# Kernel tuning notes

Measured on AMD Instinct MI355X. Metric: run time of the kernel, lower is better.

The kernel has to match this reference:

```python
import jax, jax.numpy as jnp
import numpy as np

EPS = 1e-14
RHO = 8.0


def _normalize(x):
    return x / jnp.linalg.norm(x, axis=-1, keepdims=True)


def setup_inputs() -> dict:
    key = jax.random.key(0)
    ks = jax.random.split(key, 12)
    B, D = 4096, 1024
    f = lambda k: _normalize(jax.random.normal(k, (B, D), dtype=jnp.float32))
    pos = lambda k: jax.random.uniform(k, (B, 1), dtype=jnp.float32, minval=0.1, maxval=1.0)
    return {
        "im_feat": f(ks[0]),
        "tt_feat": f(ks[1]),
        "rim_feat": f(ks[2]),
        "rtt_feat": f(ks[3]),
        "remote_u_im": pos(ks[4]),
        "remote_u_tt": pos(ks[5]),
        "loss1_im": pos(ks[6]),
        "loss1_tt": pos(ks[7]),
        "u_im": pos(ks[8]),
        "u_tt": pos(ks[9]),
        "logit_scale": 10.0 * jnp.ones((1,), dtype=jnp.float32),
        "offset": 0,
    }


def _pairwise_loss(rim, rtt, im, tt, logit_scale, offset):
    # features1 = remote, features2 = local (as in forward(): pairwise_loss(remote_features, features, ...))
    sim_image = rim @ tt.T                                  # [B1, B2]
    sim_text = rtt @ im.T                                   # [B1, B2]
    diag_sim = jnp.sum(rim * rtt, axis=-1, keepdims=True)   # [B1, 1]
    exp_im = jnp.exp((sim_image - diag_sim) * logit_scale)
    exp_tt = jnp.exp((sim_text - diag_sim) * logit_scale)
    B1, B2 = sim_image.shape
    # mask zeros the shifted diagonal: equivalent to subtracting the diagonal entry from the row sum
    cols = (jnp.arange(B1) + offset)[:, None]               # [B1, 1]
    rw_sum = B2 - 1 if B1 <= B2 else B2 * (B1 - 1) / B1
    loss_im = (jnp.sum(exp_im, axis=-1, keepdims=True)
               - jnp.take_along_axis(exp_im, cols, axis=1)) / rw_sum
    loss_tt = (jnp.sum(exp_tt, axis=-1, keepdims=True)
               - jnp.take_along_axis(exp_tt, cols, axis=1)) / rw_sum
    return loss_im, loss_tt


def reference(im_feat, tt_feat, rim_feat, rtt_feat, remote_u_im, remote_u_tt,
              loss1_im, loss1_tt, u_im, u_tt, logit_scale, offset):
    loss2_im, loss2_tt = _pairwise_loss(rim_feat, rtt_feat, im_feat, tt_feat, logit_scale, offset)
    pg1 = loss1_im / (u_im + EPS) + loss1_tt / (u_tt + EPS)
    pg2 = loss2_im / (remote_u_im + EPS) + loss2_tt / (remote_u_tt + EPS)
    loss = (jnp.mean(pg1) + jnp.mean(pg2)) / 2
    # multiply_tau branch
    ls = logit_scale[0]
    loss = loss / jax.lax.stop_gradient(ls)
    loss = loss + RHO / ls
    loss = loss + jnp.mean(jnp.log(u_im) + jnp.log(u_tt)) / 2 / ls
    return loss
```

## Files before the change

kernel.cpp:

```cpp
#include <hip/hip_runtime.h>
#include <hip/hip_bf16.h>

#define EPSF 1e-14f
#define RHOF 8.0f

typedef __attribute__((ext_vector_type(4))) float f32x4;
typedef __attribute__((ext_vector_type(2))) unsigned long long u64x2;

#define AS_GLOBAL __attribute__((address_space(1)))
#define AS_LDS    __attribute__((address_space(3)))


__global__ __launch_bounds__(256) void prep_fp8(
    const float* __restrict__ im,  const float* __restrict__ tt,
    const float* __restrict__ rim, const float* __restrict__ rtt,
    unsigned char* __restrict__ bIm,  unsigned char* __restrict__ bTt,
    unsigned char* __restrict__ bRim, unsigned char* __restrict__ bRtt,
    float* __restrict__ S_im, float* __restrict__ S_tt,
    float* __restrict__ diag, float* __restrict__ red,
    int D, int spm )
{
    __shared__ unsigned char L[8 * 1024];
    const int b = blockIdx.x;
    const int tid = threadIdx.x;
    const int nConv = 4 * spm;
    if (b < nConv) {
        int mIdx = b / spm;
        int slab = b - mIdx * spm;
        const float* src = (mIdx == 0) ? rim : (mIdx == 1) ? tt
                          : (mIdx == 2) ? rtt : im;
        unsigned char* dst = (mIdx == 0) ? bRim : (mIdx == 1) ? bTt
                            : (mIdx == 2) ? bRtt : bIm;
        const float* srow = src + (size_t)slab * 8 * D;
        const int n4 = (8 * D) >> 2;
        for (int idx = tid; idx < n4; idx += 256) {
            float4 v = *(const float4*)(srow + idx * 4);
            int pk = __builtin_amdgcn_cvt_pk_fp8_f32(v.x, v.y, 0, false);
            pk     = __builtin_amdgcn_cvt_pk_fp8_f32(v.z, v.w, pk, true);
            *(int*)&L[idx * 4] = pk;
        }
        __syncthreads();
        const int kTiles = D >> 6;
        const int rb = (slab * 8) >> 7;
        const int r0loc = (slab * 8) & 127;
        for (int g = tid; g < (D >> 1); g += 256) {
            int kb  = g >> 5;
            int rem = g & 31;
            int rl  = rem >> 2;
            int h   = rem & 3;
            int r   = slab * 8 + rl;
            int m   = (r >> 1) & 7;
            int g0  = (2 * h) ^ m;
            const unsigned char* lb = &L[rl * D + kb * 64];
            u64x2 o;
            o.x = *(const unsigned long long*)(lb + g0 * 8);
            o.y = *(const unsigned long long*)(lb + (g0 ^ 1) * 8);
            char* outp = (char*)dst
                       + ((size_t)(rb * kTiles + kb) * 512
                          + (size_t)(r0loc + rl) * 4 + h) * 16;
            *(u64x2*)outp = o;
        }
    } else {
        int db = b - nConv;
        if (db == 0 && tid < 8) red[tid] = 0.f;
        if (tid < 4) { S_im[db * 4 + tid] = 0.f; S_tt[db * 4 + tid] = 0.f; }
        int row  = db * 4 + (tid >> 6);
        int lane = tid & 63;
        const float* a = rim + (size_t)row * D;
        const float* c = rtt + (size_t)row * D;
        float s = 0.f;
        for (int k = lane * 4; k < D; k += 256) {
            float4 av = *(const float4*)(a + k);
            float4 cv = *(const float4*)(c + k);
            s += av.x * cv.x + av.y * cv.y + av.z * cv.z + av.w * cv.w;
        }
        #pragma unroll
        for (int m2 = 1; m2 < 64; m2 <<= 1) s += __shfl_xor(s, m2, 64);
        if (lane == 0) diag[row] = s;
    }
}

__global__ __launch_bounds__(256) void gemm_expsum(
    const unsigned char* __restrict__ A0, const unsigned char* __restrict__ B0,
    float* __restrict__ S0,
    const unsigned char* __restrict__ A1, const unsigned char* __restrict__ B1,
    float* __restrict__ S1,
    const float* __restrict__ logit_scale, const int* __restrict__ offset,
    int Bn, int D)
{
    const int z = blockIdx.z;
    const unsigned char* A = z ? A1 : A0;
    const unsigned char* B = z ? B1 : B0;
    float* S = z ? S1 : S0;

    __shared__ unsigned char As[8192];
    __shared__ unsigned char Bs[8192];

    const int tid  = threadIdx.x;
    const int wave = tid >> 6;
    const int lane = tid & 63;
    const int lo   = lane & 15;
    const int qd   = lane >> 4;
    const int m0   = (wave >> 1) * 64;
    const int n0   = (wave & 1) * 64;
    const int x2   = (lo >> 3) & 1;
    const int xq   = qd ^ ((lo >> 1) & 3);
    const int off0 = x2 * 32 + xq * 8;
    const int off1 = (1 - x2) * 32 + xq * 8;

    const int kTiles = D >> 6;
    const unsigned char* Atile = A + (size_t)blockIdx.y * kTiles * 8192;
    const unsigned char* Btile = B + (size_t)blockIdx.x * kTiles * 8192;

    f32x4 acc[4][4];
    #pragma unroll
    for (int i = 0; i < 4; ++i)
        #pragma unroll
        for (int j = 0; j < 4; ++j)
            acc[i][j] = (f32x4){0.f, 0.f, 0.f, 0.f};

    for (int kb = 0; kb < kTiles; ++kb) {
        #pragma unroll
        for (int j = 0; j < 4; ++j) {
            int goff = (j * 256 + tid) * 16;
            int loff = j * 4096 + wave * 1024;
            __builtin_amdgcn_global_load_lds(
                (const AS_GLOBAL unsigned int*)(Atile + goff),
                (AS_LDS unsigned int*)&As[loff], 16, 0, 0);
            __builtin_amdgcn_global_load_lds(
                (const AS_GLOBAL unsigned int*)(Btile + goff),
                (AS_LDS unsigned int*)&Bs[loff], 16, 0, 0);
        }
        __syncthreads();

        long af0[4], af1[4], bq0[4], bq1[4];
        #pragma unroll
        for (int t = 0; t < 4; ++t) {
            int ra = (m0 + 16 * t + lo) * 64;
            af0[t] = *(const long*)&As[ra + off0];
            af1[t] = *(const long*)&As[ra + off1];
            int rn = (n0 + 16 * t + lo) * 64;
            bq0[t] = *(const long*)&Bs[rn + off0];
            bq1[t] = *(const long*)&Bs[rn + off1];
        }
        #pragma unroll
        for (int ti = 0; ti < 4; ++ti)
            #pragma unroll
            for (int tj = 0; tj < 4; ++tj) {
                acc[ti][tj] = __builtin_amdgcn_mfma_f32_16x16x32_fp8_fp8(
                    af0[ti], bq0[tj], acc[ti][tj], 0, 0, 0);
                acc[ti][tj] = __builtin_amdgcn_mfma_f32_16x16x32_fp8_fp8(
                    af1[ti], bq1[tj], acc[ti][tj], 0, 0, 0);
            }
        __syncthreads();

        Atile += 8192;
        Btile += 8192;
    }

    const float ls = logit_scale[0];
    const int offs = offset[0];
    const int rowBase = blockIdx.y * 128;
    const int colBase = blockIdx.x * 128;
    #pragma unroll
    for (int ti = 0; ti < 4; ++ti) {
        #pragma unroll
        for (int r = 0; r < 4; ++r) {
            int gi = rowBase + m0 + 16 * ti + 4 * qd + r;
            float rs = 0.f;
            #pragma unroll
            for (int tj = 0; tj < 4; ++tj) {
                int gj = colBase + n0 + 16 * tj + lo;
                float e = __expf(ls * acc[ti][tj][r]);
                if (gj == gi + offs) e = 0.f;
                rs += e;
            }
            #pragma unroll
            for (int m = 1; m < 16; m <<= 1) rs += __shfl_xor(rs, m, 64);
            if (lo == 0) atomicAdd(&S[gi], rs);
        }
    }
}

__global__ __launch_bounds__(256) void final_kernel(
    const float* __restrict__ S_im, const float* __restrict__ S_tt,
    const float* __restrict__ diag,
    const float* __restrict__ ru_im, const float* __restrict__ ru_tt,
    const float* __restrict__ l1_im, const float* __restrict__ l1_tt,
    const float* __restrict__ u_im,  const float* __restrict__ u_tt,
    const float* __restrict__ logit_scale, float* __restrict__ red,
    float* __restrict__ out, int Bn)
{
    const float ls = logit_scale[0];
    const float inv_rw = 1.0f / (float)(Bn - 1);
    const int gid = blockIdx.x * 256 + threadIdx.x;
    float pg = 0.f, lg = 0.f;
    for (int i = gid; i < Bn; i += 8 * 256) {
        float p1 = l1_im[i] / (u_im[i] + EPSF) + l1_tt[i] / (u_tt[i] + EPSF);
        float dd = expf(-ls * diag[i]);
        float p2 = dd * S_im[i] * inv_rw / (ru_im[i] + EPSF)
                 + dd * S_tt[i] * inv_rw / (ru_tt[i] + EPSF);
        pg += p1 + p2;
        lg += logf(u_im[i]) + logf(u_tt[i]);
    }
    __shared__ float sp[256], sl[256];
    sp[threadIdx.x] = pg; sl[threadIdx.x] = lg;
    __syncthreads();
    for (int s = 128; s > 0; s >>= 1) {
        if (threadIdx.x < s) { sp[threadIdx.x] += sp[threadIdx.x + s];
                               sl[threadIdx.x] += sl[threadIdx.x + s]; }
        __syncthreads();
    }
    if (threadIdx.x == 0) {
        atomicAdd(&red[0], sp[0]);
        atomicAdd(&red[1], sl[0]);
        __threadfence();
        int t = atomicAdd((int*)&red[2], 1);
        if (t == gridDim.x - 1) {
            float pgSum = atomicAdd(&red[0], 0.f);
            float lgSum = atomicAdd(&red[1], 0.f);
            float loss = ((pgSum / (float)Bn) * 0.5f) / ls
                       + RHOF / ls
                       + (lgSum / (float)Bn) * 0.5f / ls;
            out[0] = loss;
        }
    }
}

extern "C" void kernel_launch(void* const* d_in, const int* in_sizes, int n_in,
                              void* d_out, int out_size, void* d_ws, size_t ws_size,
                              hipStream_t stream) {
    const float* im    = (const float*)d_in[0];
    const float* tt    = (const float*)d_in[1];
    const float* rim   = (const float*)d_in[2];
    const float* rtt   = (const float*)d_in[3];
    const float* ru_im = (const float*)d_in[4];
    const float* ru_tt = (const float*)d_in[5];
    const float* l1_im = (const float*)d_in[6];
    const float* l1_tt = (const float*)d_in[7];
    const float* u_im  = (const float*)d_in[8];
    const float* u_tt  = (const float*)d_in[9];
    const float* lsc   = (const float*)d_in[10];
    const int*   offs  = (const int*)d_in[11];

    const int Bn = in_sizes[4];
    const int D  = in_sizes[0] / Bn;
    const int spm = Bn / 8;

    char* base = (char*)d_ws;
    float* S_im = (float*)base;
    float* S_tt = S_im + Bn;
    float* diag = S_tt + Bn;
    float* red  = diag + Bn;
    const size_t headBytes = (((size_t)(3 * Bn + 8) * sizeof(float)) + 255) & ~(size_t)255;
    const size_t matBytes  = (size_t)Bn * D;
    unsigned char* buf0 = (unsigned char*)(base + headBytes);
    unsigned char* bRim = buf0;
    unsigned char* bTt  = buf0 + matBytes;
    unsigned char* bRtt = buf0 + 2 * matBytes;
    unsigned char* bIm  = buf0 + 3 * matBytes;

    prep_fp8<<<4 * spm + Bn / 4, 256, 0, stream>>>(
        im, tt, rim, rtt, bIm, bTt, bRim, bRtt, S_im, S_tt, diag, red, D, spm);

    dim3 ggrid(Bn / 128, Bn / 128, 2);
    gemm_expsum<<<ggrid, 256, 0, stream>>>(bRim, bTt, S_im, bRtt, bIm, S_tt,
                                           lsc, offs, Bn, D);

    final_kernel<<<8, 256, 0, stream>>>(S_im, S_tt, diag, ru_im, ru_tt,
                                        l1_im, l1_tt, u_im, u_tt, lsc,
                                        red, (float*)d_out, Bn);
}
```

Baseline: 200.0 us.

## Double GEMM K-tile to 128 with new fp8 swizzled packing layout

The fp8 pre-packing kernel now lays out 128-wide K tiles with a 16-way XOR swizzle, in place of 64-wide tiles. The GEMM main loop stages 16KB per operand per iteration and runs four MFMA sub-steps per tile. This halves the number of K iterations and the barriers between them. The cost is double the LDS per block, which may reduce how many blocks fit on a CU.

```diff
diff --git a/kernel.cpp b/kernel.cpp
--- a/kernel.cpp
+++ b/kernel.cpp
@@ -40,24 +40,25 @@
             *(int*)&L[idx * 4] = pk;
         }
         __syncthreads();
-        const int kTiles = D >> 6;
+        const int kTiles = D >> 7;
         const int rb = (slab * 8) >> 7;
         const int r0loc = (slab * 8) & 127;
         for (int g = tid; g < (D >> 1); g += 256) {
-            int kb  = g >> 5;
-            int rem = g & 31;
-            int rl  = rem >> 2;
-            int h   = rem & 3;
+            int kb  = g >> 6;
+            int rem = g & 63;
+            int rl  = rem >> 3;
+            int h   = rem & 7;
             int r   = slab * 8 + rl;
-            int m   = (r >> 1) & 7;
+            int m   = r & 15;
             int g0  = (2 * h) ^ m;
-            const unsigned char* lb = &L[rl * D + kb * 64];
+            int g1  = (2 * h + 1) ^ m;
+            const unsigned char* lb = &L[rl * D + kb * 128];
             u64x2 o;
             o.x = *(const unsigned long long*)(lb + g0 * 8);
-            o.y = *(const unsigned long long*)(lb + (g0 ^ 1) * 8);
+            o.y = *(const unsigned long long*)(lb + g1 * 8);
             char* outp = (char*)dst
-                       + ((size_t)(rb * kTiles + kb) * 512
-                          + (size_t)(r0loc + rl) * 4 + h) * 16;
+                       + ((size_t)(rb * kTiles + kb) * 1024
+                          + (size_t)(r0loc + rl) * 8 + h) * 16;
             *(u64x2*)outp = o;
         }
     } else {
@@ -93,8 +94,8 @@
     const unsigned char* B = z ? B1 : B0;
     float* S = z ? S1 : S0;
 
-    __shared__ unsigned char As[8192];
-    __shared__ unsigned char Bs[8192];
+    __shared__ unsigned char As[16384];
+    __shared__ unsigned char Bs[16384];
 
     const int tid  = threadIdx.x;
     const int wave = tid >> 6;
@@ -103,14 +104,13 @@
     const int qd   = lane >> 4;
     const int m0   = (wave >> 1) * 64;
     const int n0   = (wave & 1) * 64;
-    const int x2   = (lo >> 3) & 1;
-    const int xq   = qd ^ ((lo >> 1) & 3);
-    const int off0 = x2 * 32 + xq * 8;
-    const int off1 = (1 - x2) * 32 + xq * 8;
-
-    const int kTiles = D >> 6;
-    const unsigned char* Atile = A + (size_t)blockIdx.y * kTiles * 8192;
-    const unsigned char* Btile = B + (size_t)blockIdx.x * kTiles * 8192;
+    int soff[4];
+    #pragma unroll
+    for (int s = 0; s < 4; ++s) soff[s] = ((4 * s + qd) ^ lo) * 8;
+
+    const int kTiles = D >> 7;
+    const unsigned char* Atile = A + (size_t)blockIdx.y * kTiles * 16384;
+    const unsigned char* Btile = B + (size_t)blockIdx.x * kTiles * 16384;
 
     f32x4 acc[4][4];
     #pragma unroll
@@ -133,29 +133,25 @@
         }
         __syncthreads();
 
-        long af0[4], af1[4], bq0[4], bq1[4];
-        #pragma unroll
-        for (int t = 0; t < 4; ++t) {
-            int ra = (m0 + 16 * t + lo) * 64;
-            af0[t] = *(const long*)&As[ra + off0];
-            af1[t] = *(const long*)&As[ra + off1];
-            int rn = (n0 + 16 * t + lo) * 64;
-            bq0[t] = *(const long*)&Bs[rn + off0];
-            bq1[t] = *(const long*)&Bs[rn + off1];
-        }
-        #pragma unroll
-        for (int ti = 0; ti < 4; ++ti)
-            #pragma unroll
-            for (int tj = 0; tj < 4; ++tj) {
-                acc[ti][tj] = __builtin_amdgcn_mfma_f32_16x16x32_fp8_fp8(
-                    af0[ti], bq0[tj], acc[ti][tj], 0, 0, 0);
-                acc[ti][tj] = __builtin_amdgcn_mfma_f32_16x16x32_fp8_fp8(
-                    af1[ti], bq1[tj], acc[ti][tj], 0, 0, 0);
+        #pragma unroll
+        for (int s = 0; s < 4; ++s) {
+            long af[4], bq[4];
+            #pragma unroll
+            for (int t = 0; t < 4; ++t) {
+                af[t] = *(const long*)&As[(m0 + 16 * t + lo) * 128 + soff[s]];
+                bq[t] = *(const long*)&Bs[(n0 + 16 * t + lo) * 128 + soff[s]];
             }
-        __syncthreads();
-
-        Atile += 8192;
-        Btile += 8192;
+            #pragma unroll
+            for (int ti = 0; ti < 4; ++ti)
+                #pragma unroll
+                for (int tj = 0; tj < 4; ++tj)
+                    acc[ti][tj] = __builtin_amdgcn_mfma_f32_16x16x32_fp8_fp8(
+                        af[ti], bq[tj], acc[ti][tj], 0, 0, 0);
+        }
+        __syncthreads();
+
+        Atile += 16384;
+        Btile += 16384;
     }
 
     const float ls = logit_scale[0];
```

New measurement: 202.1 us. About the same (+1.1%).

## Give each wave a private LDS staging buffer and drop block barriers

Applied to the files above, without the earlier changes.

Each wave now DMA-loads its own 64-row A and B slices into a wave-private LDS region, replacing the block-wide cooperative tile load. This lets the two __syncthreads per K iteration be removed, so waves no longer stall on one another. In exchange, waves that share the same A or B rows fetch them redundantly, doubling global/L2 load traffic. LDS use also doubles to 32KB per block, which may reduce occupancy. Correctness relies on the compiler inserting the proper vmcnt waits for the async LDS loads.

```diff
diff --git a/kernel.cpp b/kernel.cpp
--- a/kernel.cpp
+++ b/kernel.cpp
@@ -93,8 +93,8 @@
     const unsigned char* B = z ? B1 : B0;
     float* S = z ? S1 : S0;
 
-    __shared__ unsigned char As[8192];
-    __shared__ unsigned char Bs[8192];
+    __shared__ unsigned char As[4][4096];
+    __shared__ unsigned char Bs[4][4096];
 
     const int tid  = threadIdx.x;
     const int wave = tid >> 6;
@@ -109,8 +109,8 @@
     const int off1 = (1 - x2) * 32 + xq * 8;
 
     const int kTiles = D >> 6;
-    const unsigned char* Atile = A + (size_t)blockIdx.y * kTiles * 8192;
-    const unsigned char* Btile = B + (size_t)blockIdx.x * kTiles * 8192;
+    const unsigned char* Ahalf = A + (size_t)blockIdx.y * kTiles * 8192 + m0 * 64;
+    const unsigned char* Bhalf = B + (size_t)blockIdx.x * kTiles * 8192 + n0 * 64;
 
     f32x4 acc[4][4];
     #pragma unroll
@@ -122,26 +122,23 @@
     for (int kb = 0; kb < kTiles; ++kb) {
         #pragma unroll
         for (int j = 0; j < 4; ++j) {
-            int goff = (j * 256 + tid) * 16;
-            int loff = j * 4096 + wave * 1024;
+            int goff = (j * 64 + lane) * 16;
             __builtin_amdgcn_global_load_lds(
-                (const AS_GLOBAL unsigned int*)(Atile + goff),
-                (AS_LDS unsigned int*)&As[loff], 16, 0, 0);
+                (const AS_GLOBAL unsigned int*)(Ahalf + goff),
+                (AS_LDS unsigned int*)&As[wave][j * 1024], 16, 0, 0);
             __builtin_amdgcn_global_load_lds(
-                (const AS_GLOBAL unsigned int*)(Btile + goff),
-                (AS_LDS unsigned int*)&Bs[loff], 16, 0, 0);
-        }
-        __syncthreads();
+                (const AS_GLOBAL unsigned int*)(Bhalf + goff),
+                (AS_LDS unsigned int*)&Bs[wave][j * 1024], 16, 0, 0);
+        }
 
         long af0[4], af1[4], bq0[4], bq1[4];
         #pragma unroll
         for (int t = 0; t < 4; ++t) {
-            int ra = (m0 + 16 * t + lo) * 64;
-            af0[t] = *(const long*)&As[ra + off0];
-            af1[t] = *(const long*)&As[ra + off1];
-            int rn = (n0 + 16 * t + lo) * 64;
-            bq0[t] = *(const long*)&Bs[rn + off0];
-            bq1[t] = *(const long*)&Bs[rn + off1];
+            int ra = (16 * t + lo) * 64;
+            af0[t] = *(const long*)&As[wave][ra + off0];
+            af1[t] = *(const long*)&As[wave][ra + off1];
+            bq0[t] = *(const long*)&Bs[wave][ra + off0];
+            bq1[t] = *(const long*)&Bs[wave][ra + off1];
         }
         #pragma unroll
         for (int ti = 0; ti < 4; ++ti)
@@ -152,10 +149,9 @@
                 acc[ti][tj] = __builtin_amdgcn_mfma_f32_16x16x32_fp8_fp8(
                     af1[ti], bq1[tj], acc[ti][tj], 0, 0, 0);
             }
-        __syncthreads();
-
-        Atile += 8192;
-        Btile += 8192;
+
+        Ahalf += 8192;
+        Bhalf += 8192;
     }
 
     const float ls = logit_scale[0];
```

After: 208.8 us. +4.4%, slower.
